# Optimization experiments

Measured on AMD Instinct MI355X. Metric: run time of the kernel, lower is better.

The kernel has to match this reference:

```python
import jax, jax.numpy as jnp
import numpy as np

B, S, D = 4, 4096, 64   # batch, seq_len, input_size
H, HD = 4, 16           # num_heads, head_dim


def setup_inputs() -> dict:
    key = jax.random.key(0)
    ks = jax.random.split(key, 9)
    sd = 1.0 / np.sqrt(D)          # torch Linear default uniform(-1/sqrt(fan_in), ...)
    so = 1.0 / np.sqrt(H * HD)
    u = lambda k, shape, s: jax.random.uniform(k, shape, jnp.float32, -s, s)
    return {
        "x": jax.random.normal(ks[0], (B, S, D), jnp.float32),
        "Wq": u(ks[1], (H, D, HD), sd), "bq": u(ks[2], (H, HD), sd),
        "Wk": u(ks[3], (H, D, HD), sd), "bk": u(ks[4], (H, HD), sd),
        "Wv": u(ks[5], (H, D, HD), sd), "bv": u(ks[6], (H, HD), sd),
        "Wo": u(ks[7], (H * HD, D), so), "bo": u(ks[8], (D,), so),
    }


def reference(x, Wq, bq, Wk, bk, Wv, bv, Wo, bo):
    # Batched per-head projections (fuses the original per-head Linear loop)
    q = jnp.einsum('bsd,hde->bhse', x, Wq) + bq[None, :, None, :]
    k = jnp.einsum('bsd,hde->bhse', x, Wk) + bk[None, :, None, :]
    v = jnp.einsum('bsd,hde->bhse', x, Wv) + bv[None, :, None, :]
    # scores: [B, H, S(query), S(key)]
    scores = jnp.einsum('bhse,bhte->bhst', q, k) / np.sqrt(HD).astype(np.float32)
    # FAITHFUL quirk: torch Softmax(dim=1) on [B,S,S] normalizes over the QUERY axis
    w = jax.nn.softmax(scores, axis=2)
    attended = jnp.einsum('bhst,bhte->bhse', w, v)          # [B,H,S,HD]
    concat = attended.transpose(0, 2, 1, 3).reshape(B, S, H * HD)
    out = concat @ Wo + bo                                   # [B,S,D]
    # FAITHFUL quirk: final softmax over the sequence axis (dim=1)
    return jax.nn.softmax(out, axis=1)
```

## Files before the change

### kernel.cpp

```cpp
#include <hip/hip_runtime.h>
#include <hip/hip_bf16.h>


#define BB 4
#define SS 4096
#define DD 64
#define HH 4
#define HDD 16

typedef unsigned int u32;
typedef unsigned short u16;
typedef __attribute__((ext_vector_type(8))) short bfrag;
typedef __attribute__((ext_vector_type(4))) float floatx4;
typedef __attribute__((ext_vector_type(16))) float floatx16;
typedef __attribute__((ext_vector_type(2))) u32 u32x2;
typedef __attribute__((ext_vector_type(4))) u32 u32x4;

#define LOG2E 1.4426950408889634074f
#define QSCALE (LOG2E * 0.25f)

__device__ __forceinline__ float fexp2(float x) {
#if __has_builtin(__builtin_amdgcn_exp2f)
  return __builtin_amdgcn_exp2f(x);
#else
  float r; asm("v_exp_f32 %0, %1" : "=v"(r) : "v"(x)); return r;
#endif
}
__device__ __forceinline__ float frcp(float x) {
#if __has_builtin(__builtin_amdgcn_rcpf)
  return __builtin_amdgcn_rcpf(x);
#else
  float r; asm("v_rcp_f32 %0, %1" : "=v"(r) : "v"(x)); return r;
#endif
}

__device__ __forceinline__ u16 f2bf(float f) {
  u32 u = __builtin_bit_cast(u32, f);
  return (u16)((u + 0x7FFFu + ((u >> 16) & 1u)) >> 16);
}
__device__ __forceinline__ u32 pack_bf(float lo, float hi) {
#if __has_builtin(__builtin_amdgcn_perm)
  return __builtin_amdgcn_perm(__builtin_bit_cast(u32, hi),
                               __builtin_bit_cast(u32, lo), 0x07060302u);
#else
  u32 a = __builtin_bit_cast(u32, lo);
  u32 b = __builtin_bit_cast(u32, hi);
  return (a >> 16) | (b & 0xFFFF0000u);
#endif
}

__device__ __forceinline__ void gload_lds16(const u16* g, u16* l) {
  __builtin_amdgcn_global_load_lds(
      (const __attribute__((address_space(1))) void*)(g),
      (__attribute__((address_space(3))) void*)(l), 16, 0, 0);
}

__device__ __forceinline__ int tmap(int c) {
  int c5 = c & 31;
  return (c & ~31) + (c5 & 3) + ((c5 >> 2) & 1) * 8 + ((c5 >> 3) & 1) * 16
       + ((c5 >> 4) & 1) * 4;
}

__global__ __launch_bounds__(256) void k_proj(
    const float* __restrict__ x,
    const float* __restrict__ Wq, const float* __restrict__ bq,
    const float* __restrict__ Wk, const float* __restrict__ bk,
    const float* __restrict__ Wv, const float* __restrict__ bv,
    u16* __restrict__ qb, u16* __restrict__ kb, float* __restrict__ vf)
{
  __shared__ float xs[16 * 64];
  const int tid = threadIdx.x;
  const int blk = blockIdx.x;
  const int b   = blk >> 8;
  const int s0  = (blk & 255) << 4;
  ((float4*)xs)[tid] = ((const float4*)(x + ((size_t)b * SS + s0) * DD))[tid];
  __syncthreads();

  const int col = tid & 63, h = col >> 4, e = col & 15;
  const int rg  = tid >> 6;
  float aq[4] = {0,0,0,0}, ak[4] = {0,0,0,0}, av[4] = {0,0,0,0};
  const int wofs = h * (DD * HDD) + e;
#pragma unroll 4
  for (int d = 0; d < DD; ++d) {
    float wq = Wq[wofs + d * HDD];
    float wk = Wk[wofs + d * HDD];
    float wv = Wv[wofs + d * HDD];
    const float* xr = xs + (rg * 4) * 64 + d;
#pragma unroll
    for (int r = 0; r < 4; ++r) {
      float xv = xr[r * 64];
      aq[r] += xv * wq; ak[r] += xv * wk; av[r] += xv * wv;
    }
  }
  const float bqv = bq[col], bkv = bk[col], bvv = bv[col];
  size_t base = ((size_t)(b * HH + h) * SS + (s0 + rg * 4)) * HDD + e;
#pragma unroll
  for (int r = 0; r < 4; ++r) {
    qb[base + r * HDD] = f2bf((aq[r] + bqv) * QSCALE);
    kb[base + r * HDD] = f2bf(ak[r] + bkv);
    vf[base + r * HDD] = av[r] + bvv;
  }
}

__global__ __launch_bounds__(256, 4) void k_csvp(
    const u16* __restrict__ qb, const u16* __restrict__ kb,
    const float* __restrict__ vf, u16* __restrict__ vp)
{
  __shared__ float vstage[128 * 16];
  __shared__ float rcl[128];
  const int tid = threadIdx.x;
  const int lane = tid & 63, w = tid >> 6;
  const int l31 = lane & 31, hl = lane >> 5;
  const int bx = blockIdx.x;
  const int bh = blockIdx.y;
  const int t0 = bx * 128 + w * 32;
  const size_t base = (size_t)bh * (SS * HDD);

  {
    const float4* vsrc4 = (const float4*)(vf + ((size_t)bh * SS + bx * 128) * HDD);
    ((float4*)vstage)[tid]       = vsrc4[tid];
    ((float4*)vstage)[tid + 256] = vsrc4[tid + 256];
  }

  const bfrag kf = *(const bfrag*)(kb + base + (size_t)(t0 + l31) * HDD + hl * 8);
  const u16* qpc = qb + base + (size_t)l31 * HDD + hl * 8;
  const floatx16 z16 = {0.f};
  float c0 = 0.f, c1 = 0.f, c2 = 0.f, c3 = 0.f;

#define LQ(i) (*(const bfrag*)(qpc + (size_t)(i) * (32 * HDD)))
#define ACCUM(dv)                                   \
  do {                                              \
    _Pragma("unroll")                               \
    for (int j = 0; j < 4; ++j) {                   \
      c0 += fexp2((dv)[4 * j + 0]);                 \
      c1 += fexp2((dv)[4 * j + 1]);                 \
      c2 += fexp2((dv)[4 * j + 2]);                 \
      c3 += fexp2((dv)[4 * j + 3]);                 \
    }                                               \
  } while (0)

  bfrag q0 = LQ(0), q1 = LQ(1), q2v = LQ(2), q3 = LQ(3);
#pragma unroll 1
  for (int o = 0; o < 4; ++o) {
#pragma unroll
    for (int i = 0; i < 32; i += 4) {
      {
        floatx16 d = __builtin_amdgcn_mfma_f32_32x32x16_bf16(q0, kf, z16, 0, 0, 0);
        q0 = LQ(i + 4);  ACCUM(d);
      }
      {
        floatx16 d = __builtin_amdgcn_mfma_f32_32x32x16_bf16(q1, kf, z16, 0, 0, 0);
        q1 = LQ(i + 5);  ACCUM(d);
      }
      {
        floatx16 d = __builtin_amdgcn_mfma_f32_32x32x16_bf16(q2v, kf, z16, 0, 0, 0);
        q2v = LQ(i + 6); ACCUM(d);
      }
      {
        floatx16 d = __builtin_amdgcn_mfma_f32_32x32x16_bf16(q3, kf, z16, 0, 0, 0);
        q3 = LQ(i + 7);  ACCUM(d);
      }
    }
    qpc += 32 * 32 * HDD;
  }
#undef LQ
#undef ACCUM

  float c = (c0 + c1) + (c2 + c3);
  c += __shfl_xor(c, 32, 64);
  if (hl == 0)
    rcl[w * 32 + l31] = frcp(c);
  __syncthreads();

  const int e = tid >> 4;
  const int h0 = bx & 1;
  const int poff = h0 * 16 + (tid & 15);
  const int cc = poff ^ (e & 7);
  const int h128 = h0 * 128;
  u32 r[4];
#pragma unroll
  for (int jj = 0; jj < 4; ++jj) {
    int ta = tmap(cc * 8 + 2 * jj)     - h128;
    int tb = tmap(cc * 8 + 2 * jj + 1) - h128;
    u16 lo = f2bf(vstage[ta * 16 + e] * rcl[ta]);
    u16 hi = f2bf(vstage[tb * 16 + e] * rcl[tb]);
    r[jj] = (u32)lo | ((u32)hi << 16);
  }
  u16* outb = vp + ((size_t)bh * 16 + (bx >> 1)) * 4096;
  u32x4 vv = {r[0], r[1], r[2], r[3]};
  *(u32x4*)(outb + e * 256 + poff * 8) = vv;
}

__global__ __launch_bounds__(256, 4) void k_attn(
    const u16* __restrict__ qb, const u16* __restrict__ kb,
    const u16* __restrict__ vp, float* __restrict__ attp)
{
  __shared__ __align__(16) u16 vls[2][4096];
  const int tid  = threadIdx.x;
  const int lane = tid & 63, w = tid >> 6;
  const int l31 = lane & 31, hl = lane >> 5;
  const int bh = blockIdx.z, b = bh >> 2, h = bh & 3;
  const int tph = blockIdx.y;
  const int s0 = blockIdx.x * 128 + w * 32;
  const size_t base = (size_t)bh * (SS * HDD);

  const bfrag qf = *(const bfrag*)(qb + base + (size_t)(s0 + l31) * HDD + hl * 8);
  const u16* kp = kb + base + ((size_t)tph * 2048 + l31) * HDD + hl * 8;
  const floatx16 z16 = {0.f};
  floatx16 acc = {0.f};

  const u16* vsrc = vp + ((size_t)bh * 16 + tph * 8) * 4096;

  {
    const u16* gs = vsrc + w * 1024 + lane * 8;
    u16* ls = &vls[0][0] + w * 1024;
    gload_lds16(gs, ls);
    gload_lds16(gs + 512, ls + 512);
  }
  bfrag kfr[8];
#pragma unroll
  for (int it = 0; it < 8; ++it)
    kfr[it] = *(const bfrag*)(kp + (size_t)(it * 32) * HDD);
  __syncthreads();

#pragma unroll
  for (int ch = 0; ch < 8; ++ch) {
    if (ch < 7) {
      const u16* gs = vsrc + (ch + 1) * 4096 + w * 1024 + lane * 8;
      u16* ls = &vls[(ch + 1) & 1][0] + w * 1024;
      gload_lds16(gs, ls);
      gload_lds16(gs + 512, ls + 512);
    }

    const u16* vrow = &vls[ch & 1][0] + (l31 & 15) * 256;
    const int eb = l31 & 7;
#pragma unroll
    for (int it = 0; it < 8; ++it) {
      bfrag kf = kfr[it];
      if (ch < 7)
        kfr[it] = *(const bfrag*)(kp + (size_t)((ch + 1) * 256 + it * 32) * HDD);
      floatx16 d = __builtin_amdgcn_mfma_f32_32x32x16_bf16(kf, qf, z16, 0, 0, 0);
      u32 wr[8];
#pragma unroll
      for (int p = 0; p < 8; ++p)
        wr[p] = pack_bf(fexp2(d[2 * p]), fexp2(d[2 * p + 1]));
      const int cc0 = it * 4 + hl * 2;
      u32x4 af0 = *(const u32x4*)(vrow + ((cc0 ^ eb) << 3));
      u32x4 af1 = *(const u32x4*)(vrow + (((cc0 + 1) ^ eb) << 3));
      u32x4 ef0 = {wr[0], wr[1], wr[2], wr[3]};
      u32x4 ef1 = {wr[4], wr[5], wr[6], wr[7]};
      acc = __builtin_amdgcn_mfma_f32_32x32x16_bf16(
          __builtin_bit_cast(bfrag, af0), __builtin_bit_cast(bfrag, ef0), acc, 0, 0, 0);
      acc = __builtin_amdgcn_mfma_f32_32x32x16_bf16(
          __builtin_bit_cast(bfrag, af1), __builtin_bit_cast(bfrag, ef1), acc, 0, 0, 0);
    }
    __syncthreads();
  }

  float* ao = attp + (((size_t)tph * BB + b) * SS + s0 + l31) * (HH * HDD)
            + h * HDD + 4 * hl;
  float4 lo4 = {acc[0], acc[1], acc[2], acc[3]};
  float4 hi4 = {acc[4], acc[5], acc[6], acc[7]};
  *(float4*)ao       = lo4;
  *(float4*)(ao + 8) = hi4;
}

__global__ __launch_bounds__(256) void k_oproj(
    const float* __restrict__ att, const float* __restrict__ Wo,
    const float* __restrict__ bo, float* __restrict__ outp,
    float* __restrict__ part)
{
  __shared__ float wols[64 * 64];
  __shared__ float red[4][64];
  const int tid = threadIdx.x;
  const int blk = blockIdx.x;
  const int b = blk >> 9, s0 = (blk & 511) << 3;
#pragma unroll
  for (int i = 0; i < 4; ++i)
    ((float4*)wols)[tid + 256 * i] = ((const float4*)Wo)[tid + 256 * i];
  __syncthreads();

  const int d = tid & 63, sg = tid >> 6;
  const float bov = bo[d];
  const size_t so = (size_t)BB * SS * 16;
  float es = 0.f;
#pragma unroll
  for (int r = 0; r < 2; ++r) {
    int s = s0 + sg * 2 + r;
    const floatx4* row = (const floatx4*)(att + ((size_t)b * SS + s) * 64);
    float acc = bov;
#pragma unroll
    for (int j = 0; j < 16; ++j) {
      floatx4 c = row[j] + row[j + so];
      acc += c[0] * wols[(4*j+0)*64 + d] + c[1] * wols[(4*j+1)*64 + d]
           + c[2] * wols[(4*j+2)*64 + d] + c[3] * wols[(4*j+3)*64 + d];
    }
    outp[((size_t)b * SS + s) * 64 + d] = acc;
    es += fexp2(acc * LOG2E);
  }
  red[sg][d] = es;
  __syncthreads();
  if (tid < 64)
    part[((size_t)b * 512 + (blk & 511)) * 64 + tid] =
        red[0][tid] + red[1][tid] + red[2][tid] + red[3][tid];
}

__global__ __launch_bounds__(256) void k_softmax(
    const float* __restrict__ outp, const float* __restrict__ part,
    float* __restrict__ out)
{
  __shared__ float red[4][64];
  __shared__ float rs[64];
  const int tid = threadIdx.x, d = tid & 63, sg = tid >> 6;
  const int st = blockIdx.x;
  const int b = blockIdx.y;
  {
    float e = 0.f;
    const float* pp = part + ((size_t)b * 512 + sg * 128) * 64 + d;
#pragma unroll 8
    for (int c = 0; c < 128; ++c) e += pp[c * 64];
    red[sg][d] = e;
  }
  __syncthreads();
  if (tid < 64)
    rs[tid] = frcp(red[0][tid] + red[1][tid] + red[2][tid] + red[3][tid]);
  __syncthreads();
  const float r = rs[d];
  const size_t rowbase = ((size_t)b * SS + st * 64 + sg * 16) * 64 + d;
#pragma unroll 4
  for (int i = 0; i < 16; ++i)
    out[rowbase + i * 64] = fexp2(outp[rowbase + i * 64] * LOG2E) * r;
}

extern "C" void kernel_launch(void* const* d_in, const int* in_sizes, int n_in,
                              void* d_out, int out_size, void* d_ws, size_t ws_size,
                              hipStream_t stream) {
  const float* x  = (const float*)d_in[0];
  const float* Wq = (const float*)d_in[1];
  const float* bq = (const float*)d_in[2];
  const float* Wk = (const float*)d_in[3];
  const float* bk = (const float*)d_in[4];
  const float* Wv = (const float*)d_in[5];
  const float* bv = (const float*)d_in[6];
  const float* Wo = (const float*)d_in[7];
  const float* bo = (const float*)d_in[8];

  char* ws = (char*)d_ws;
  constexpr size_t QB_OFF  = 0;
  constexpr size_t KB_OFF  = (size_t)2  << 20;
  constexpr size_t VF_OFF  = (size_t)4  << 20;
  constexpr size_t VP_OFF  = (size_t)8  << 20;
  constexpr size_t ATT_OFF = (size_t)10 << 20;
  constexpr size_t OUT_OFF = (size_t)18 << 20;
  constexpr size_t PT_OFF  = (size_t)22 << 20;

  u16*   qb   = (u16*)  (ws + QB_OFF);
  u16*   kb   = (u16*)  (ws + KB_OFF);
  float* vf   = (float*)(ws + VF_OFF);
  u16*   vpb  = (u16*)  (ws + VP_OFF);
  float* attp = (float*)(ws + ATT_OFF);
  float* outp = (float*)(ws + OUT_OFF);
  float* part = (float*)(ws + PT_OFF);
  float* out  = (float*)d_out;

  hipLaunchKernelGGL(k_proj,    dim3(1024),       dim3(256), 0, stream,
                     x, Wq, bq, Wk, bk, Wv, bv, qb, kb, vf);
  hipLaunchKernelGGL(k_csvp,    dim3(32, 16),     dim3(256), 0, stream,
                     qb, kb, vf, vpb);
  hipLaunchKernelGGL(k_attn,    dim3(32, 2, 16),  dim3(256), 0, stream,
                     qb, kb, vpb, attp);
  hipLaunchKernelGGL(k_oproj,   dim3(2048),       dim3(256), 0, stream,
                     attp, Wo, bo, outp, part);
  hipLaunchKernelGGL(k_softmax, dim3(64, 4),      dim3(256), 0, stream, outp, part, out);
}
```

Measured before the change: 184.7 us.

## Split csvp query sweep across two wave groups and pipeline QK MFMA ahead of exp

k_csvp now launches 512 threads per block. Two groups of four waves each sweep half of the query axis, and their partial column sums are combined in shared memory before the reciprocal is taken. This doubles the waves available to hide the exp-heavy column-sum loop. In both k_csvp and k_attn, the score MFMA for the next tile is issued before the exp2 and accumulate work on the current tile, so matrix-core latency can overlap with VALU work. The cost is an extra block barrier, more live registers from holding two score tiles, and one extra speculative q load past the end of each half.

```diff
diff --git a/kernel.cpp b/kernel.cpp
--- a/kernel.cpp
+++ b/kernel.cpp
@@ -102,28 +102,29 @@
   }
 }
 
-__global__ __launch_bounds__(256, 4) void k_csvp(
+__global__ __launch_bounds__(512, 4) void k_csvp(
     const u16* __restrict__ qb, const u16* __restrict__ kb,
     const float* __restrict__ vf, u16* __restrict__ vp)
 {
   __shared__ float vstage[128 * 16];
+  __shared__ float cpart[2][128];
   __shared__ float rcl[128];
   const int tid = threadIdx.x;
   const int lane = tid & 63, w = tid >> 6;
   const int l31 = lane & 31, hl = lane >> 5;
   const int bx = blockIdx.x;
   const int bh = blockIdx.y;
-  const int t0 = bx * 128 + w * 32;
+  const int t0 = bx * 128 + (w & 3) * 32;
+  const int shalf = w >> 2;
   const size_t base = (size_t)bh * (SS * HDD);
 
   {
     const float4* vsrc4 = (const float4*)(vf + ((size_t)bh * SS + bx * 128) * HDD);
-    ((float4*)vstage)[tid]       = vsrc4[tid];
-    ((float4*)vstage)[tid + 256] = vsrc4[tid + 256];
+    ((float4*)vstage)[tid] = vsrc4[tid];
   }
 
   const bfrag kf = *(const bfrag*)(kb + base + (size_t)(t0 + l31) * HDD + hl * 8);
-  const u16* qpc = qb + base + (size_t)l31 * HDD + hl * 8;
+  const u16* qpc = qb + base + ((size_t)shalf * 2048 + l31) * HDD + hl * 8;
   const floatx16 z16 = {0.f};
   float c0 = 0.f, c1 = 0.f, c2 = 0.f, c3 = 0.f;
 
@@ -138,57 +139,60 @@
       c3 += fexp2((dv)[4 * j + 3]);                 \
     }                                               \
   } while (0)
+#define STEP(qr, ri)                                                        \
+  do {                                                                      \
+    floatx16 dB = __builtin_amdgcn_mfma_f32_32x32x16_bf16(qr, kf, z16, 0, 0, 0); \
+    qr = LQ(ri);                                                            \
+    ACCUM(dA);                                                              \
+    dA = dB;                                                                \
+  } while (0)
 
   bfrag q0 = LQ(0), q1 = LQ(1), q2v = LQ(2), q3 = LQ(3);
+  floatx16 dA = __builtin_amdgcn_mfma_f32_32x32x16_bf16(q0, kf, z16, 0, 0, 0);
+  q0 = LQ(4);
 #pragma unroll 1
-  for (int o = 0; o < 4; ++o) {
+  for (int o = 0; o < 2; ++o) {
 #pragma unroll
     for (int i = 0; i < 32; i += 4) {
-      {
-        floatx16 d = __builtin_amdgcn_mfma_f32_32x32x16_bf16(q0, kf, z16, 0, 0, 0);
-        q0 = LQ(i + 4);  ACCUM(d);
-      }
-      {
-        floatx16 d = __builtin_amdgcn_mfma_f32_32x32x16_bf16(q1, kf, z16, 0, 0, 0);
-        q1 = LQ(i + 5);  ACCUM(d);
-      }
-      {
-        floatx16 d = __builtin_amdgcn_mfma_f32_32x32x16_bf16(q2v, kf, z16, 0, 0, 0);
-        q2v = LQ(i + 6); ACCUM(d);
-      }
-      {
-        floatx16 d = __builtin_amdgcn_mfma_f32_32x32x16_bf16(q3, kf, z16, 0, 0, 0);
-        q3 = LQ(i + 7);  ACCUM(d);
-      }
+      STEP(q1,  i + 5);
+      STEP(q2v, i + 6);
+      STEP(q3,  i + 7);
+      STEP(q0,  i + 8);
     }
     qpc += 32 * 32 * HDD;
   }
+#undef STEP
 #undef LQ
 #undef ACCUM
 
   float c = (c0 + c1) + (c2 + c3);
   c += __shfl_xor(c, 32, 64);
   if (hl == 0)
-    rcl[w * 32 + l31] = frcp(c);
-  __syncthreads();
-
-  const int e = tid >> 4;
-  const int h0 = bx & 1;
-  const int poff = h0 * 16 + (tid & 15);
-  const int cc = poff ^ (e & 7);
-  const int h128 = h0 * 128;
-  u32 r[4];
-#pragma unroll
-  for (int jj = 0; jj < 4; ++jj) {
-    int ta = tmap(cc * 8 + 2 * jj)     - h128;
-    int tb = tmap(cc * 8 + 2 * jj + 1) - h128;
-    u16 lo = f2bf(vstage[ta * 16 + e] * rcl[ta]);
-    u16 hi = f2bf(vstage[tb * 16 + e] * rcl[tb]);
-    r[jj] = (u32)lo | ((u32)hi << 16);
-  }
-  u16* outb = vp + ((size_t)bh * 16 + (bx >> 1)) * 4096;
-  u32x4 vv = {r[0], r[1], r[2], r[3]};
-  *(u32x4*)(outb + e * 256 + poff * 8) = vv;
+    cpart[shalf][(w & 3) * 32 + l31] = c;
+  __syncthreads();
+  if (tid < 128)
+    rcl[tid] = frcp(cpart[0][tid] + cpart[1][tid]);
+  __syncthreads();
+
+  if (tid < 256) {
+    const int e = tid >> 4;
+    const int h0 = bx & 1;
+    const int poff = h0 * 16 + (tid & 15);
+    const int cc = poff ^ (e & 7);
+    const int h128 = h0 * 128;
+    u32 r[4];
+#pragma unroll
+    for (int jj = 0; jj < 4; ++jj) {
+      int ta = tmap(cc * 8 + 2 * jj)     - h128;
+      int tb = tmap(cc * 8 + 2 * jj + 1) - h128;
+      u16 lo = f2bf(vstage[ta * 16 + e] * rcl[ta]);
+      u16 hi = f2bf(vstage[tb * 16 + e] * rcl[tb]);
+      r[jj] = (u32)lo | ((u32)hi << 16);
+    }
+    u16* outb = vp + ((size_t)bh * 16 + (bx >> 1)) * 4096;
+    u32x4 vv = {r[0], r[1], r[2], r[3]};
+    *(u32x4*)(outb + e * 256 + poff * 8) = vv;
+  }
 }
 
 __global__ __launch_bounds__(256, 4) void k_attn(
@@ -221,6 +225,7 @@
 #pragma unroll
   for (int it = 0; it < 8; ++it)
     kfr[it] = *(const bfrag*)(kp + (size_t)(it * 32) * HDD);
+  floatx16 dA = __builtin_amdgcn_mfma_f32_32x32x16_bf16(kfr[0], qf, z16, 0, 0, 0);
   __syncthreads();
 
 #pragma unroll
@@ -236,14 +241,19 @@
     const int eb = l31 & 7;
 #pragma unroll
     for (int it = 0; it < 8; ++it) {
-      bfrag kf = kfr[it];
       if (ch < 7)
         kfr[it] = *(const bfrag*)(kp + (size_t)((ch + 1) * 256 + it * 32) * HDD);
-      floatx16 d = __builtin_amdgcn_mfma_f32_32x32x16_bf16(kf, qf, z16, 0, 0, 0);
+      floatx16 dB;
+      if (ch == 7 && it == 7) {
+        dB = dA;
+      } else {
+        bfrag kn = (it < 7) ? kfr[it + 1] : kfr[0];
+        dB = __builtin_amdgcn_mfma_f32_32x32x16_bf16(kn, qf, z16, 0, 0, 0);
+      }
       u32 wr[8];
 #pragma unroll
       for (int p = 0; p < 8; ++p)
-        wr[p] = pack_bf(fexp2(d[2 * p]), fexp2(d[2 * p + 1]));
+        wr[p] = pack_bf(fexp2(dA[2 * p]), fexp2(dA[2 * p + 1]));
       const int cc0 = it * 4 + hl * 2;
       u32x4 af0 = *(const u32x4*)(vrow + ((cc0 ^ eb) << 3));
       u32x4 af1 = *(const u32x4*)(vrow + (((cc0 + 1) ^ eb) << 3));
@@ -253,6 +263,7 @@
           __builtin_bit_cast(bfrag, af0), __builtin_bit_cast(bfrag, ef0), acc, 0, 0, 0);
       acc = __builtin_amdgcn_mfma_f32_32x32x16_bf16(
           __builtin_bit_cast(bfrag, af1), __builtin_bit_cast(bfrag, ef1), acc, 0, 0, 0);
+      dA = dB;
     }
     __syncthreads();
   }
@@ -365,7 +376,7 @@
 
   hipLaunchKernelGGL(k_proj,    dim3(1024),       dim3(256), 0, stream,
                      x, Wq, bq, Wk, bk, Wv, bv, qb, kb, vf);
-  hipLaunchKernelGGL(k_csvp,    dim3(32, 16),     dim3(256), 0, stream,
+  hipLaunchKernelGGL(k_csvp,    dim3(32, 16),     dim3(512), 0, stream,
                      qb, kb, vf, vpb);
   hipLaunchKernelGGL(k_attn,    dim3(32, 2, 16),  dim3(256), 0, stream,
                      qb, kb, vpb, attp);
```

New measurement: 183.0 us. No clear change (-0.9%).
